# Kernel optimization log

Measured on AMD Instinct MI355X. Metric: run time of the kernel, lower is better.

Reference implementation:

```python
import jax, jax.numpy as jnp
import numpy as np

N_HEAD = 16

def _proj(W, b, x):
    # 1x1 Conv2d: x is (b, e, h, w) -> (b, o, h, w)
    return jnp.einsum('oe,behw->bohw', W, x) + b[None, :, None, None]

def setup_inputs() -> dict:
    key = jax.random.key(0)
    ks = jax.random.split(key, 12)
    B, E, S = 2, 1024, 2048
    d_qk, d_v, d_out = E, E, E
    def xavier(k, o, i):
        bound = np.sqrt(6.0 / (o + i))
        return jax.random.uniform(k, (o, i), jnp.float32, -bound, bound)
    return {
        'q': jax.random.normal(ks[0], (B, E, 1, S), jnp.float32),
        'k': jax.random.normal(ks[1], (B, E, 1, S), jnp.float32),
        'v': jax.random.normal(ks[2], (B, E, 1, S), jnp.float32),
        'qk_mask': jax.random.normal(ks[3], (B, S, 1, S), jnp.float32),
        'Wq': xavier(ks[4], d_qk, E), 'bq': jnp.zeros((d_qk,), jnp.float32),
        'Wk': xavier(ks[5], d_qk, E), 'bk': jnp.zeros((d_qk,), jnp.float32),
        'Wv': xavier(ks[6], d_v, E), 'bv': jnp.zeros((d_v,), jnp.float32),
        'Wo': xavier(ks[7], d_out, d_v), 'bo': jnp.zeros((d_out,), jnp.float32),
    }

def reference(q, k, v, qk_mask, Wq, bq, Wk, bk, Wv, bv, Wo, bo):
    # q,k,v: (B, E, 1, S); qk_mask: (B, S_src, 1, S_tgt)
    qp = _proj(Wq, bq, q)
    kp = _proj(Wk, bk, k)
    vp = _proj(Wv, bv, v)
    B, C, _, S = qp.shape
    H = N_HEAD
    dh = C // H
    scale = float(dh) ** -0.5
    qh = (qp * scale).reshape(B, H, dh, S)   # (b, h, c, q)
    kh = kp.reshape(B, H, dh, S)             # (b, h, c, k)
    vh = vp.reshape(B, H, dh, S)             # (b, h, c, k)
    # per-head scores, equivalent to the split einsum 'bchq,bkhc->bkhq'
    scores = jnp.einsum('bhcq,bhck->bhkq', qh, kh)        # (b, h, k, q)
    scores = scores + qk_mask[:, None, :, 0, :]           # mask broadcast over heads
    w = jax.nn.softmax(scores, axis=2)                    # softmax over key dim (dim=1 per-head)
    attn = jnp.einsum('bhkq,bhck->bhcq', w, vh).reshape(B, C, 1, S)
    return _proj(Wo, bo, attn)
```

## Files before the change

kernel.cpp:

```cpp
#include <hip/hip_runtime.h>
#include <hip/hip_bf16.h>

typedef unsigned short ushort_t;
typedef __attribute__((ext_vector_type(8))) __bf16 bf16x8;
typedef __attribute__((ext_vector_type(4))) float f32x4;
typedef __attribute__((ext_vector_type(2))) unsigned int u32x2;
typedef __attribute__((ext_vector_type(8))) unsigned short us8;

#define DEV __device__ __forceinline__

constexpr int BB = 2, EE = 1024, SS = 2048, HH = 16;
constexpr float L2E = 1.44269504088896f;
constexpr float SCALE_Q = 0.125f * 1.44269504088896f;

DEV ushort_t f2bf(float x) {
  union { float f; unsigned u; } c; c.f = x;
  unsigned u = c.u;
  return (ushort_t)((u + 0x7fffu + ((u >> 16) & 1u)) >> 16);
}

DEV unsigned cvtpk(float lo, float hi) {
  unsigned r;
  asm volatile("v_cvt_pk_bf16_f32 %0, %1, %2" : "=v"(r) : "v"(lo), "v"(hi));
  return r;
}

DEV void gload16(const void* g, void* l) {
  __builtin_amdgcn_global_load_lds((const __attribute__((address_space(1))) void*)g,
                                   (__attribute__((address_space(3))) void*)l, 16, 0, 0);
}

struct TpArgs { const float* i0; const float* i1; const float* i2;
                ushort_t* o0; ushort_t* o1; ushort_t* o2; };

__global__ __launch_bounds__(256) void k_transpose_cvt(TpArgs a) {
  int z = blockIdx.z; int p = z >> 1; int b = z & 1;
  const float* in = (p == 0) ? a.i0 : (p == 1) ? a.i1 : a.i2;
  ushort_t* out = (p == 0) ? a.o0 : (p == 1) ? a.o1 : a.o2;
  in += (long long)b * EE * SS;
  out += (long long)b * SS * EE;
  int s0 = blockIdx.x * 64, e0 = blockIdx.y * 64;
  __shared__ __align__(16) ushort_t T[64][72];
  int t = threadIdx.x;
  int sc = (t & 15) * 4, erb = t >> 4;
#pragma unroll
  for (int it = 0; it < 4; ++it) {
    int er = erb + it * 16;
    float4 v = *(const float4*)(in + (long long)(e0 + er) * SS + s0 + sc);
    T[sc + 0][er] = f2bf(v.x);
    T[sc + 1][er] = f2bf(v.y);
    T[sc + 2][er] = f2bf(v.z);
    T[sc + 3][er] = f2bf(v.w);
  }
  __syncthreads();
#pragma unroll
  for (int it = 0; it < 2; ++it) {
    int slot = t + it * 256;
    int sr = slot >> 3, ec = (slot & 7) * 8;
    us8 v = *(const us8*)&T[sr][ec];
    *(us8*)(out + (long long)(s0 + sr) * EE + e0 + ec) = v;
  }
}

struct WArgs { const float* w0; const float* w1; const float* w2; const float* w3;
               ushort_t* o0; ushort_t* o1; ushort_t* o2; ushort_t* o3; };

__global__ __launch_bounds__(256) void k_cvt_w(WArgs a) {
  int y = blockIdx.y;
  const float* in = (y == 0) ? a.w0 : (y == 1) ? a.w1 : (y == 2) ? a.w2 : a.w3;
  ushort_t* out = (y == 0) ? a.o0 : (y == 1) ? a.o1 : (y == 2) ? a.o2 : a.o3;
  long long idx = ((long long)blockIdx.x * 256 + threadIdx.x) * 4;
  float4 v = *(const float4*)(in + idx);
  unsigned lo = f2bf(v.x) | ((unsigned)f2bf(v.y) << 16);
  unsigned hi = f2bf(v.z) | ((unsigned)f2bf(v.w) << 16);
  u32x2 pk = {lo, hi};
  *(u32x2*)(out + idx) = pk;
}

DEV void stage_tile(const ushort_t* src0, ushort_t* dst0, int w, int lane) {
#pragma unroll
  for (int i = 0; i < 2; ++i) {
    int u = w * 128 + i * 64 + lane;
    int row = u >> 2, part = u & 3;
    gload16(src0 + (long long)row * 1024 + part * 8, dst0 + (w * 128 + i * 64) * 8);
  }
}

__global__ __launch_bounds__(256) void k_proj(
    const ushort_t* __restrict__ xq, const ushort_t* __restrict__ xk,
    const ushort_t* __restrict__ xv, const ushort_t* __restrict__ wq,
    const ushort_t* __restrict__ wk, const ushort_t* __restrict__ wv,
    const float* __restrict__ bqp, const float* __restrict__ bkp,
    const float* __restrict__ bvp,
    ushort_t* __restrict__ qpT, ushort_t* __restrict__ kpT,
    ushort_t* __restrict__ vpN) {
  constexpr int K = 1024;
  __shared__ __align__(16) ushort_t As[2][4096];
  __shared__ __align__(16) ushort_t Bs[2][4096];
  int t = threadIdx.x, lane = t & 63, w = t >> 6;
  int lq = lane & 15, g = lane >> 4;
  int z = blockIdx.z, pair = z >> 1, b = z & 1;
  long long s2 = (long long)SS * EE;
  int m0, n0, LDo; bool browq; float scale; const float* bias;
  const ushort_t *Ab, *Bb; ushort_t* Co;
  if (pair < 2) {
    m0 = blockIdx.y * 128; n0 = blockIdx.x * 128;
    Ab = (pair == 0 ? wq : wk) + (long long)m0 * K;
    Bb = (pair == 0 ? xq : xk) + b * s2 + (long long)n0 * K;
    Co = (pair == 0 ? qpT : kpT) + b * s2;
    bias = (pair == 0 ? bqp : bkp);
    scale = (pair == 0 ? SCALE_Q : 1.0f);
    LDo = EE; browq = true;
  } else {
    m0 = blockIdx.x * 128; n0 = blockIdx.y * 128;
    Ab = xv + b * s2 + (long long)m0 * K;
    Bb = wv + (long long)n0 * K;
    Co = vpN + b * s2;
    bias = bvp; scale = 1.0f; LDo = SS; browq = false;
  }

  f32x4 acc[4][4];
#pragma unroll
  for (int mi = 0; mi < 4; ++mi)
#pragma unroll
    for (int ni = 0; ni < 4; ++ni) acc[mi][ni] = (f32x4){0.f, 0.f, 0.f, 0.f};

  stage_tile(Ab, As[0], w, lane);
  stage_tile(Bb, Bs[0], w, lane);
  __syncthreads();
  int wm = w >> 1, wn = w & 1;
  for (int kt = 0; kt < K / 32; ++kt) {
    int buf = kt & 1;
    if (kt + 1 < K / 32) {
      stage_tile(Ab + (kt + 1) * 32, As[buf ^ 1], w, lane);
      stage_tile(Bb + (kt + 1) * 32, Bs[buf ^ 1], w, lane);
    }
    bf16x8 aF[4], bF[4];
#pragma unroll
    for (int mi = 0; mi < 4; ++mi)
      aF[mi] = *(const bf16x8*)&As[buf][(wm * 64 + mi * 16 + lq) * 32 + g * 8];
#pragma unroll
    for (int ni = 0; ni < 4; ++ni)
      bF[ni] = *(const bf16x8*)&Bs[buf][(wn * 64 + ni * 16 + lq) * 32 + g * 8];
#pragma unroll
    for (int mi = 0; mi < 4; ++mi)
#pragma unroll
      for (int ni = 0; ni < 4; ++ni)
        acc[mi][ni] = __builtin_amdgcn_mfma_f32_16x16x32_bf16(aF[mi], bF[ni], acc[mi][ni], 0, 0, 0);
    __syncthreads();
  }
#pragma unroll
  for (int ni = 0; ni < 4; ++ni) {
    int col = n0 + wn * 64 + ni * 16 + lq;
    float bc = browq ? 0.f : bias[col];
#pragma unroll
    for (int mi = 0; mi < 4; ++mi) {
      int row0 = m0 + wm * 64 + mi * 16 + 4 * g;
      f32x4 v = acc[mi][ni];
#pragma unroll
      for (int r = 0; r < 4; ++r) {
        float bb = browq ? bias[row0 + r] : bc;
        v[r] = (v[r] + bb) * scale;
      }
      u32x2 pk = {cvtpk(v[0], v[1]), cvtpk(v[2], v[3])};
      *(u32x2*)(Co + (long long)col * LDo + row0) = pk;
    }
  }
}

__global__ __launch_bounds__(256) void k_gemm_out(
    const ushort_t* __restrict__ A, long long sA,
    const ushort_t* __restrict__ Bm,
    float* __restrict__ C, long long sC,
    const float* __restrict__ bias, int LDo) {
  constexpr int K = 1024;
  __shared__ __align__(16) ushort_t As[2][4096];
  __shared__ __align__(16) ushort_t Bs[2][4096];
  int t = threadIdx.x, lane = t & 63, w = t >> 6;
  int lq = lane & 15, g = lane >> 4;
  int m0 = blockIdx.y * 128, n0 = blockIdx.x * 128;
  const ushort_t* Ab = A + (long long)blockIdx.z * sA + (long long)m0 * K;
  const ushort_t* Bb = Bm + (long long)n0 * K;

  f32x4 acc[4][4];
#pragma unroll
  for (int mi = 0; mi < 4; ++mi)
#pragma unroll
    for (int ni = 0; ni < 4; ++ni) acc[mi][ni] = (f32x4){0.f, 0.f, 0.f, 0.f};

  stage_tile(Ab, As[0], w, lane);
  stage_tile(Bb, Bs[0], w, lane);
  __syncthreads();
  int wm = w >> 1, wn = w & 1;
  for (int kt = 0; kt < K / 32; ++kt) {
    int buf = kt & 1;
    if (kt + 1 < K / 32) {
      stage_tile(Ab + (kt + 1) * 32, As[buf ^ 1], w, lane);
      stage_tile(Bb + (kt + 1) * 32, Bs[buf ^ 1], w, lane);
    }
    bf16x8 aF[4], bF[4];
#pragma unroll
    for (int mi = 0; mi < 4; ++mi)
      aF[mi] = *(const bf16x8*)&As[buf][(wm * 64 + mi * 16 + lq) * 32 + g * 8];
#pragma unroll
    for (int ni = 0; ni < 4; ++ni)
      bF[ni] = *(const bf16x8*)&Bs[buf][(wn * 64 + ni * 16 + lq) * 32 + g * 8];
#pragma unroll
    for (int mi = 0; mi < 4; ++mi)
#pragma unroll
      for (int ni = 0; ni < 4; ++ni)
        acc[mi][ni] = __builtin_amdgcn_mfma_f32_16x16x32_bf16(aF[mi], bF[ni], acc[mi][ni], 0, 0, 0);
    __syncthreads();
  }
#pragma unroll
  for (int ni = 0; ni < 4; ++ni) {
    int col = n0 + wn * 64 + ni * 16 + lq;
    float bc = bias[col];
#pragma unroll
    for (int mi = 0; mi < 4; ++mi) {
      int row0 = m0 + wm * 64 + mi * 16 + 4 * g;
      f32x4 v = acc[mi][ni];
#pragma unroll
      for (int r = 0; r < 4; ++r) v[r] += bc;
      *(f32x4*)(C + (long long)blockIdx.z * sC + (long long)col * LDo + row0) = v;
    }
  }
}

__global__ __launch_bounds__(256, 4) void k_attn(
    const ushort_t* __restrict__ qpT, const ushort_t* __restrict__ kpT,
    const ushort_t* __restrict__ vp, const float* __restrict__ mask,
    ushort_t* __restrict__ attnT) {
  int t = threadIdx.x, lane = t & 63, w = t >> 6;
  int lq = lane & 15, g = lane >> 4;
  int sw = lq >> 2;
  int kvsw = lq & 7;
  int qt = blockIdx.x, h = blockIdx.y, b = blockIdx.z;
  int q0 = qt * 64;
  long long s2 = (long long)SS * EE;
  const ushort_t* qT = qpT + b * s2;
  const ushort_t* kTb = kpT + b * s2 + h * 64;
  const ushort_t* vB = vp + b * s2 + (long long)(h * 64) * SS;
  const float* mk = mask + (long long)b * SS * SS;
  ushort_t* aT = attnT + b * s2;

  __shared__ __align__(16) ushort_t Kt[2][4096];
  __shared__ __align__(16) ushort_t Vt[2][4096];
  __shared__ __align__(16) ushort_t Pt[4][1024];

  int qglob = q0 + w * 16;
  const float* mbase = mk + qglob + lq;

  bf16x8 qF[2];
#pragma unroll
  for (int ch = 0; ch < 2; ++ch)
    qF[ch] = *(const bf16x8*)(qT + (long long)(qglob + lq) * EE + h * 64 + ch * 32 + g * 8);

  int srow = (lane >> 3);
  int sslot = lane & 7;
  auto stageKV = [&](int buf, int k0) {
#pragma unroll
    for (int i = 0; i < 2; ++i) {
      int row = w * 16 + i * 8 + srow;
      int ps = sslot ^ (row & 7);
      gload16(kTb + (long long)(k0 + row) * EE + ps * 8,
              &Kt[buf][(w * 16 + i * 8) * 64]);
      gload16(vB + (long long)row * SS + k0 + ps * 8,
              &Vt[buf][(w * 16 + i * 8) * 64]);
    }
  };

  stageKV(0, 0);
  float mv[4][4];
#pragma unroll
  for (int kf = 0; kf < 4; ++kf)
#pragma unroll
    for (int r = 0; r < 4; ++r)
      mv[kf][r] = mbase[(long long)(kf * 16 + 4 * g + r) * SS];
  __syncthreads();

  f32x4 accO[4];
#pragma unroll
  for (int cf = 0; cf < 4; ++cf) accO[cf] = (f32x4){0.f, 0.f, 0.f, 0.f};
  float mrun = -3e38f, lrun = 0.f;

#pragma unroll 1
  for (int kt = 0; kt < SS / 64; ++kt) {
    int k0 = kt * 64;
    int cur = kt & 1;
    if (kt + 1 < SS / 64) stageKV(cur ^ 1, k0 + 64);

    f32x4 accS[4];
#pragma unroll
    for (int kf = 0; kf < 4; ++kf) accS[kf] = (f32x4){0.f, 0.f, 0.f, 0.f};
    __builtin_amdgcn_s_setprio(1);
#pragma unroll
    for (int ch = 0; ch < 2; ++ch) {
      bf16x8 aK[4];
#pragma unroll
      for (int kf = 0; kf < 4; ++kf) {
        int row = kf * 16 + lq;
        aK[kf] = *(const bf16x8*)&Kt[cur][row * 64 + (((ch * 4 + g) ^ kvsw) * 8)];
      }
#pragma unroll
      for (int kf = 0; kf < 4; ++kf)
        accS[kf] = __builtin_amdgcn_mfma_f32_16x16x32_bf16(aK[kf], qF[ch], accS[kf], 0, 0, 0);
    }
    __builtin_amdgcn_s_setprio(0);

    float sv[4][4];
    float tm = -3e38f;
#pragma unroll
    for (int kf = 0; kf < 4; ++kf)
#pragma unroll
      for (int r = 0; r < 4; ++r) {
        sv[kf][r] = fmaf(mv[kf][r], L2E, accS[kf][r]);
        tm = fmaxf(tm, sv[kf][r]);
      }
    tm = fmaxf(tm, __shfl_xor(tm, 16));
    tm = fmaxf(tm, __shfl_xor(tm, 32));
    if (__any(tm > mrun + 8.0f)) {
      float mnew = fmaxf(mrun, tm);
      float corr = __builtin_amdgcn_exp2f(mrun - mnew);
      lrun *= corr;
#pragma unroll
      for (int cf = 0; cf < 4; ++cf) accO[cf] = accO[cf] * corr;
      mrun = mnew;
    }
    if (kt + 1 < SS / 64) {
#pragma unroll
      for (int kf = 0; kf < 4; ++kf)
#pragma unroll
        for (int r = 0; r < 4; ++r)
          mv[kf][r] = mbase[(long long)(k0 + 64 + kf * 16 + 4 * g + r) * SS];
    }
    float ps = 0.f;
    unsigned pk0[4], pk1[4];
#pragma unroll
    for (int kf = 0; kf < 4; ++kf) {
      float p0 = __builtin_amdgcn_exp2f(sv[kf][0] - mrun);
      float p1 = __builtin_amdgcn_exp2f(sv[kf][1] - mrun);
      float p2 = __builtin_amdgcn_exp2f(sv[kf][2] - mrun);
      float p3 = __builtin_amdgcn_exp2f(sv[kf][3] - mrun);
      ps += (p0 + p1) + (p2 + p3);
      pk0[kf] = cvtpk(p0, p1);
      pk1[kf] = cvtpk(p2, p3);
    }
    ps += __shfl_xor(ps, 16);
    ps += __shfl_xor(ps, 32);
    lrun += ps;
#pragma unroll
    for (int kf = 0; kf < 4; ++kf) {
      int slot = ((kf & 1) * 2 + (g >> 1)) ^ sw;
      u32x2 pkv = {pk0[kf], pk1[kf]};
      *(u32x2*)&Pt[w][(kf >> 1) * 512 + lq * 32 + slot * 8 + (g & 1) * 4] = pkv;
    }

    __builtin_amdgcn_s_setprio(1);
#pragma unroll
    for (int ch = 0; ch < 2; ++ch) {
      bf16x8 bP = *(const bf16x8*)&Pt[w][ch * 512 + lq * 32 + (g ^ sw) * 8];
#pragma unroll
      for (int cf = 0; cf < 4; ++cf) {
        int row = cf * 16 + lq;
        bf16x8 vF = *(const bf16x8*)&Vt[cur][row * 64 + (((ch * 4 + g) ^ kvsw) * 8)];
        accO[cf] = __builtin_amdgcn_mfma_f32_16x16x32_bf16(vF, bP, accO[cf], 0, 0, 0);
      }
    }
    __builtin_amdgcn_s_setprio(0);
    __syncthreads();
  }

  float inv = 1.f / lrun;
  int s = qglob + lq;
#pragma unroll
  for (int cf = 0; cf < 4; ++cf) {
    int c0 = h * 64 + cf * 16 + 4 * g;
    f32x4 v = accO[cf];
    u32x2 pk = {cvtpk(v[0] * inv, v[1] * inv), cvtpk(v[2] * inv, v[3] * inv)};
    *(u32x2*)(aT + (long long)s * EE + c0) = pk;
  }
}

extern "C" void kernel_launch(void* const* d_in, const int* in_sizes, int n_in,
                              void* d_out, int out_size, void* d_ws, size_t ws_size,
                              hipStream_t stream) {
  const float* q = (const float*)d_in[0];
  const float* k = (const float*)d_in[1];
  const float* v = (const float*)d_in[2];
  const float* mask = (const float*)d_in[3];
  const float* Wq = (const float*)d_in[4];
  const float* bq = (const float*)d_in[5];
  const float* Wk = (const float*)d_in[6];
  const float* bk = (const float*)d_in[7];
  const float* Wv = (const float*)d_in[8];
  const float* bv = (const float*)d_in[9];
  const float* Wo = (const float*)d_in[10];
  const float* bo = (const float*)d_in[11];
  float* out = (float*)d_out;

  char* ws = (char*)d_ws;
  const long long MB = 1024LL * 1024LL;
  ushort_t* xqT = (ushort_t*)(ws + 0 * MB);
  ushort_t* xkT = (ushort_t*)(ws + 8 * MB);
  ushort_t* xvT = (ushort_t*)(ws + 16 * MB);
  ushort_t* wqB = (ushort_t*)(ws + 24 * MB);
  ushort_t* wkB = (ushort_t*)(ws + 26 * MB);
  ushort_t* wvB = (ushort_t*)(ws + 28 * MB);
  ushort_t* woB = (ushort_t*)(ws + 30 * MB);
  ushort_t* qpT = (ushort_t*)(ws + 32 * MB);
  ushort_t* kpT = (ushort_t*)(ws + 40 * MB);
  ushort_t* vpN = (ushort_t*)(ws + 48 * MB);
  ushort_t* anT = (ushort_t*)(ws + 56 * MB);

  TpArgs tp{q, k, v, xqT, xkT, xvT};
  hipLaunchKernelGGL(k_transpose_cvt, dim3(SS / 64, EE / 64, 6), dim3(256), 0, stream, tp);
  WArgs wa{Wq, Wk, Wv, Wo, wqB, wkB, wvB, woB};
  hipLaunchKernelGGL(k_cvt_w, dim3(1024, 4, 1), dim3(256), 0, stream, wa);

  hipLaunchKernelGGL(k_proj, dim3(SS / 128, EE / 128, 6), dim3(256), 0, stream,
                     xqT, xkT, xvT, wqB, wkB, wvB, bq, bk, bv, qpT, kpT, vpN);
  hipLaunchKernelGGL(k_attn, dim3(SS / 64, HH, BB), dim3(256), 0, stream,
                     qpT, kpT, vpN, mask, anT);
  long long s2 = (long long)SS * EE;
  hipLaunchKernelGGL(k_gemm_out, dim3(EE / 128, SS / 128, BB), dim3(256), 0, stream,
                     anT, s2, woB, out, s2, bo, SS);
}
```

Measured before the change: 165.2 us.

## Split attention over key halves with 512-thread blocks and a combine kernel

Measured after the change: 361.3 us. +118.8%, slower.

```diff
diff --git a/kernel.cpp b/kernel.cpp
--- a/kernel.cpp
+++ b/kernel.cpp
@@ -227,26 +227,27 @@
   }
 }
 
-__global__ __launch_bounds__(256, 4) void k_attn(
+__global__ __launch_bounds__(512, 8) void k_attn(
     const ushort_t* __restrict__ qpT, const ushort_t* __restrict__ kpT,
     const ushort_t* __restrict__ vp, const float* __restrict__ mask,
-    ushort_t* __restrict__ attnT) {
+    float* __restrict__ Op, float* __restrict__ ml) {
   int t = threadIdx.x, lane = t & 63, w = t >> 6;
   int lq = lane & 15, g = lane >> 4;
   int sw = lq >> 2;
   int kvsw = lq & 7;
-  int qt = blockIdx.x, h = blockIdx.y, b = blockIdx.z;
-  int q0 = qt * 64;
+  int qt = blockIdx.x, h = blockIdx.y, z = blockIdx.z;
+  int b = z & 1, sp = z >> 1;
+  int q0 = qt * 128;
+  int ksta = sp * (SS / 2);
   long long s2 = (long long)SS * EE;
   const ushort_t* qT = qpT + b * s2;
   const ushort_t* kTb = kpT + b * s2 + h * 64;
   const ushort_t* vB = vp + b * s2 + (long long)(h * 64) * SS;
   const float* mk = mask + (long long)b * SS * SS;
-  ushort_t* aT = attnT + b * s2;
 
   __shared__ __align__(16) ushort_t Kt[2][4096];
   __shared__ __align__(16) ushort_t Vt[2][4096];
-  __shared__ __align__(16) ushort_t Pt[4][1024];
+  __shared__ __align__(16) ushort_t Pt[8][512];
 
   int qglob = q0 + w * 16;
   const float* mbase = mk + qglob + lq;
@@ -256,27 +257,22 @@
   for (int ch = 0; ch < 2; ++ch)
     qF[ch] = *(const bf16x8*)(qT + (long long)(qglob + lq) * EE + h * 64 + ch * 32 + g * 8);
 
-  int srow = (lane >> 3);
+  int srow = lane >> 3;
   int sslot = lane & 7;
   auto stageKV = [&](int buf, int k0) {
-#pragma unroll
-    for (int i = 0; i < 2; ++i) {
-      int row = w * 16 + i * 8 + srow;
-      int ps = sslot ^ (row & 7);
-      gload16(kTb + (long long)(k0 + row) * EE + ps * 8,
-              &Kt[buf][(w * 16 + i * 8) * 64]);
-      gload16(vB + (long long)row * SS + k0 + ps * 8,
-              &Vt[buf][(w * 16 + i * 8) * 64]);
-    }
+    int row = w * 8 + srow;
+    int ps = sslot ^ srow;
+    gload16(kTb + (long long)(k0 + row) * EE + ps * 8, &Kt[buf][w * 512]);
+    gload16(vB + (long long)row * SS + k0 + ps * 8, &Vt[buf][w * 512]);
   };
 
-  stageKV(0, 0);
+  stageKV(0, ksta);
   float mv[4][4];
 #pragma unroll
   for (int kf = 0; kf < 4; ++kf)
 #pragma unroll
     for (int r = 0; r < 4; ++r)
-      mv[kf][r] = mbase[(long long)(kf * 16 + 4 * g + r) * SS];
+      mv[kf][r] = mbase[(long long)(ksta + kf * 16 + 4 * g + r) * SS];
   __syncthreads();
 
   f32x4 accO[4];
@@ -285,10 +281,10 @@
   float mrun = -3e38f, lrun = 0.f;
 
 #pragma unroll 1
-  for (int kt = 0; kt < SS / 64; ++kt) {
-    int k0 = kt * 64;
+  for (int kt = 0; kt < SS / 2 / 64; ++kt) {
+    int k0 = ksta + kt * 64;
     int cur = kt & 1;
-    if (kt + 1 < SS / 64) stageKV(cur ^ 1, k0 + 64);
+    if (kt + 1 < SS / 2 / 64) stageKV(cur ^ 1, k0 + 64);
 
     f32x4 accS[4];
 #pragma unroll
@@ -317,6 +313,13 @@
         sv[kf][r] = fmaf(mv[kf][r], L2E, accS[kf][r]);
         tm = fmaxf(tm, sv[kf][r]);
       }
+    if (kt + 1 < SS / 2 / 64) {
+#pragma unroll
+      for (int kf = 0; kf < 4; ++kf)
+#pragma unroll
+        for (int r = 0; r < 4; ++r)
+          mv[kf][r] = mbase[(long long)(k0 + 64 + kf * 16 + 4 * g + r) * SS];
+    }
     tm = fmaxf(tm, __shfl_xor(tm, 16));
     tm = fmaxf(tm, __shfl_xor(tm, 32));
     if (__any(tm > mrun + 8.0f)) {
@@ -326,13 +329,6 @@
 #pragma unroll
       for (int cf = 0; cf < 4; ++cf) accO[cf] = accO[cf] * corr;
       mrun = mnew;
-    }
-    if (kt + 1 < SS / 64) {
-#pragma unroll
-      for (int kf = 0; kf < 4; ++kf)
-#pragma unroll
-        for (int r = 0; r < 4; ++r)
-          mv[kf][r] = mbase[(long long)(k0 + 64 + kf * 16 + 4 * g + r) * SS];
     }
     float ps = 0.f;
     unsigned pk0[4], pk1[4];
@@ -349,17 +345,17 @@
     ps += __shfl_xor(ps, 16);
     ps += __shfl_xor(ps, 32);
     lrun += ps;
-#pragma unroll
-    for (int kf = 0; kf < 4; ++kf) {
-      int slot = ((kf & 1) * 2 + (g >> 1)) ^ sw;
-      u32x2 pkv = {pk0[kf], pk1[kf]};
-      *(u32x2*)&Pt[w][(kf >> 1) * 512 + lq * 32 + slot * 8 + (g & 1) * 4] = pkv;
-    }
 
     __builtin_amdgcn_s_setprio(1);
 #pragma unroll
     for (int ch = 0; ch < 2; ++ch) {
-      bf16x8 bP = *(const bf16x8*)&Pt[w][ch * 512 + lq * 32 + (g ^ sw) * 8];
+#pragma unroll
+      for (int kf = 2 * ch; kf < 2 * ch + 2; ++kf) {
+        int slot = ((kf & 1) * 2 + (g >> 1)) ^ sw;
+        u32x2 pkv = {pk0[kf], pk1[kf]};
+        *(u32x2*)&Pt[w][lq * 32 + slot * 8 + (g & 1) * 4] = pkv;
+      }
+      bf16x8 bP = *(const bf16x8*)&Pt[w][lq * 32 + (g ^ sw) * 8];
 #pragma unroll
       for (int cf = 0; cf < 4; ++cf) {
         int row = cf * 16 + lq;
@@ -371,15 +367,41 @@
     __syncthreads();
   }
 
-  float inv = 1.f / lrun;
   int s = qglob + lq;
+  long long obase = ((long long)(sp * 2 + b) * SS + s) * EE;
 #pragma unroll
   for (int cf = 0; cf < 4; ++cf) {
     int c0 = h * 64 + cf * 16 + 4 * g;
-    f32x4 v = accO[cf];
-    u32x2 pk = {cvtpk(v[0] * inv, v[1] * inv), cvtpk(v[2] * inv, v[3] * inv)};
-    *(u32x2*)(aT + (long long)s * EE + c0) = pk;
-  }
+    *(f32x4*)(Op + obase + c0) = accO[cf];
+  }
+  if (g == 0) {
+    float2 v2 = {mrun, lrun};
+    *(float2*)(ml + (((long long)(sp * 2 + b) * HH + h) * SS + s) * 2) = v2;
+  }
+}
+
+__global__ __launch_bounds__(256) void k_combine(
+    const float* __restrict__ Op, const float* __restrict__ ml,
+    ushort_t* __restrict__ anT) {
+  long long idx = (long long)blockIdx.x * 256 + threadIdx.x;
+  long long e = idx * 4;
+  int c = (int)(e & 1023);
+  int s = (int)((e >> 10) & 2047);
+  int b = (int)(e >> 21);
+  int h = c >> 6;
+  const float2* mlp = (const float2*)ml;
+  float2 ml0 = mlp[((long long)b * HH + h) * SS + s];
+  float2 ml1 = mlp[((long long)(2 + b) * HH + h) * SS + s];
+  float M = fmaxf(ml0.x, ml1.x);
+  float w0 = __builtin_amdgcn_exp2f(ml0.x - M);
+  float w1 = __builtin_amdgcn_exp2f(ml1.x - M);
+  float inv = 1.f / fmaf(ml0.y, w0, ml1.y * w1);
+  w0 *= inv; w1 *= inv;
+  f32x4 O0 = *(const f32x4*)(Op + ((long long)b * SS + s) * EE + c);
+  f32x4 O1 = *(const f32x4*)(Op + ((long long)(2 + b) * SS + s) * EE + c);
+  f32x4 o = O0 * w0 + O1 * w1;
+  u32x2 pk = {cvtpk(o[0], o[1]), cvtpk(o[2], o[3])};
+  *(u32x2*)(anT + (long long)b * SS * EE + (long long)s * EE + c) = pk;
 }
 
 extern "C" void kernel_launch(void* const* d_in, const int* in_sizes, int n_in,
@@ -401,17 +423,19 @@
 
   char* ws = (char*)d_ws;
   const long long MB = 1024LL * 1024LL;
+  float*    Opb = (float*)(ws + 0 * MB);
   ushort_t* xqT = (ushort_t*)(ws + 0 * MB);
   ushort_t* xkT = (ushort_t*)(ws + 8 * MB);
   ushort_t* xvT = (ushort_t*)(ws + 16 * MB);
   ushort_t* wqB = (ushort_t*)(ws + 24 * MB);
   ushort_t* wkB = (ushort_t*)(ws + 26 * MB);
   ushort_t* wvB = (ushort_t*)(ws + 28 * MB);
-  ushort_t* woB = (ushort_t*)(ws + 30 * MB);
-  ushort_t* qpT = (ushort_t*)(ws + 32 * MB);
-  ushort_t* kpT = (ushort_t*)(ws + 40 * MB);
-  ushort_t* vpN = (ushort_t*)(ws + 48 * MB);
-  ushort_t* anT = (ushort_t*)(ws + 56 * MB);
+  float*    mlb = (float*)(ws + 32 * MB);
+  ushort_t* woB = (ushort_t*)(ws + 33 * MB);
+  ushort_t* qpT = (ushort_t*)(ws + 35 * MB);
+  ushort_t* kpT = (ushort_t*)(ws + 43 * MB);
+  ushort_t* vpN = (ushort_t*)(ws + 51 * MB);
+  ushort_t* anT = (ushort_t*)(ws + 59 * MB);
 
   TpArgs tp{q, k, v, xqT, xkT, xvT};
   hipLaunchKernelGGL(k_transpose_cvt, dim3(SS / 64, EE / 64, 6), dim3(256), 0, stream, tp);
@@ -420,8 +444,9 @@
 
   hipLaunchKernelGGL(k_proj, dim3(SS / 128, EE / 128, 6), dim3(256), 0, stream,
                      xqT, xkT, xvT, wqB, wkB, wvB, bq, bk, bv, qpT, kpT, vpN);
-  hipLaunchKernelGGL(k_attn, dim3(SS / 64, HH, BB), dim3(256), 0, stream,
-                     qpT, kpT, vpN, mask, anT);
+  hipLaunchKernelGGL(k_attn, dim3(SS / 128, HH, BB * 2), dim3(512), 0, stream,
+                     qpT, kpT, vpN, mask, Opb, mlb);
+  hipLaunchKernelGGL(k_combine, dim3(4096), dim3(256), 0, stream, Opb, mlb, anT);
   long long s2 = (long long)SS * EE;
   hipLaunchKernelGGL(k_gemm_out, dim3(EE / 128, SS / 128, BB), dim3(256), 0, stream,
                      anT, s2, woB, out, s2, bo, SS);
```
